# Kernel tuning notes

Hardware: AMD Instinct MI355X
Metric: run time of the kernel (lower is better)

## Reference

```python
import jax, jax.numpy as jnp
import numpy as np

N, F, H, T, E, HOR = 50000, 24, 128, 12, 800000, 6


def setup_inputs() -> dict:
    key = jax.random.key(0)
    ks = jax.random.split(key, 16)
    x_seq = jax.random.normal(ks[0], (T, N, F), jnp.float32)
    ei_seq = jax.random.randint(ks[1], (T, 2, E), 0, N, jnp.int32)
    ea_seq = jax.random.uniform(ks[2], (T, E), jnp.float32)
    mask_seq = jax.random.bernoulli(ks[3], 0.9, (T, N))
    s = 1.0 / float(np.sqrt(H))
    def w(k, shape):
        return jax.random.uniform(k, shape, jnp.float32, -s, s)
    params = dict(
        Wz=w(ks[4], (F, H)), Wr=w(ks[5], (F, H)), Wh=w(ks[6], (F, H)),
        bz=jnp.zeros((H,), jnp.float32), br=jnp.zeros((H,), jnp.float32), bh=jnp.zeros((H,), jnp.float32),
        LWz=w(ks[7], (2 * H, H)), LWr=w(ks[8], (2 * H, H)), LWh=w(ks[9], (2 * H, H)),
        Lbz=w(ks[10], (H,)), Lbr=w(ks[11], (H,)), Lbh=w(ks[12], (H,)),
        headW=w(ks[13], (H, F)), headb=w(ks[14], (F,)),
    )
    return dict(x_seq=x_seq, ei_seq=ei_seq, ea_seq=ea_seq, mask_seq=mask_seq, id_seq=0, **params)


def _gcn(x, src, dst, ew, W, b):
    xw = x @ W                                                     # [N,H]
    deg = jnp.zeros((x.shape[0],), xw.dtype).at[dst].add(ew) + 1.0  # in-degree + self-loop
    dinv = jax.lax.rsqrt(deg)
    coef = dinv[src] * ew * dinv[dst]                              # [E]
    agg = jnp.zeros_like(xw).at[dst].add(xw[src] * coef[:, None])
    return agg + xw * (1.0 / deg)[:, None] + b                     # normalized self-loop term


def _cell(x, src, dst, ew, h, p):
    # TGCN (GCN-GRU) cell from pytorch_geometric_temporal
    z = jax.nn.sigmoid(jnp.concatenate([_gcn(x, src, dst, ew, p['Wz'], p['bz']), h], 1) @ p['LWz'] + p['Lbz'])
    r = jax.nn.sigmoid(jnp.concatenate([_gcn(x, src, dst, ew, p['Wr'], p['br']), h], 1) @ p['LWr'] + p['Lbr'])
    htil = jnp.tanh(jnp.concatenate([_gcn(x, src, dst, ew, p['Wh'], p['bh']), h * r], 1) @ p['LWh'] + p['Lbh'])
    return z * h + (1.0 - z) * htil


def _forward(x_seq, ei_seq, ea_seq, mask_seq, p):
    Nn, Hh = x_seq.shape[1], p['LWz'].shape[1]

    # Encoder over T steps: h_store keeps last hidden of every node ever present
    def enc(carry, inp):
        h_store, seen = carry
        x, ei, ew, mask = inp
        h_prev = jnp.where((mask & seen)[:, None], h_store, 0.0)
        h_new = _cell(x, ei[0], ei[1], ew, h_prev, p)
        return (jnp.where(mask[:, None], h_new, h_store), seen | mask), None

    init = (jnp.zeros((Nn, Hh), x_seq.dtype), jnp.zeros((Nn,), bool))
    (h_store, seen), _ = jax.lax.scan(enc, init, (x_seq, ei_seq, ea_seq, mask_seq))

    h_prev = jnp.where((mask_seq[-1] & seen)[:, None], h_store, 0.0)
    src_l, dst_l, ew_l = ei_seq[-1, 0], ei_seq[-1, 1], ea_seq[-1]

    def dec(carry, _):
        h, inp = carry
        h_new = _cell(inp, src_l, dst_l, ew_l, h, p)
        y = h_new @ p['headW'] + p['headb']
        return (h_new, y), y

    _, preds = jax.lax.scan(dec, (h_prev, x_seq[-1]), None, length=HOR)
    return preds  # [horizon, N, out_channels]


def reference(x_seq, ei_seq, ea_seq, mask_seq, id_seq, Wz, Wr, Wh, bz, br, bh,
              LWz, LWr, LWh, Lbz, Lbr, Lbh, headW, headb):
    p = dict(Wz=Wz, Wr=Wr, Wh=Wh, bz=bz, br=br, bh=bh,
             LWz=LWz, LWr=LWr, LWh=LWh, Lbz=Lbz, Lbr=Lbr, Lbh=Lbh,
             headW=headW, headb=headb)
    return _forward(x_seq, ei_seq, ea_seq, mask_seq, p)
```

## Files before the change

### kernel.cpp

```cpp
#include <hip/hip_runtime.h>

#define NN 50000
#define FF 24
#define HH 128
#define TT 12
#define EE 800000
#define HORZ 6


__global__ void k_maskdetect(const unsigned char* __restrict__ m, int* __restrict__ flag) {
    int i = blockIdx.x * 256 + threadIdx.x;
    if (i < 16384 && (i & 3) != 0 && m[i] != 0) atomicOr(flag, 1);
}

__global__ void k_maskconv(const unsigned char* __restrict__ mraw, const int* __restrict__ flag,
                           unsigned char* __restrict__ mout) {
    int i = blockIdx.x * 256 + threadIdx.x;
    if (i >= TT * NN) return;
    if (*flag) mout[i] = (mraw[i] != 0);
    else       mout[i] = (((const int*)mraw)[i] != 0);
}


__global__ void k_hist(const int* __restrict__ ei, int* __restrict__ cnt,
                       int* __restrict__ rank) {
    int idx = blockIdx.x * 256 + threadIdx.x;
    if (idx >= TT * EE) return;
    int t = idx / EE, e = idx - t * EE;
    int dst = ei[((size_t)t * 2 + 1) * EE + e];
    rank[idx] = atomicAdd(&cnt[t * NN + dst], 1);
}

__global__ void k_scan(const int* __restrict__ cnt, int* __restrict__ offs) {
    __shared__ int sums[1024];
    int t = blockIdx.x, tid = threadIdx.x;
    const int per = (NN + 1023) / 1024;
    int base = tid * per;
    int s = 0;
    for (int i = 0; i < per; i++) {
        int idx = base + i;
        if (idx < NN) s += cnt[t * NN + idx];
    }
    sums[tid] = s;
    __syncthreads();
    for (int off = 1; off < 1024; off <<= 1) {
        int tv = (tid >= off) ? sums[tid - off] : 0;
        __syncthreads();
        sums[tid] += tv;
        __syncthreads();
    }
    int run = sums[tid] - s;
    for (int i = 0; i < per; i++) {
        int idx = base + i;
        if (idx < NN) {
            offs[t * (NN + 1) + idx] = run;
            run += cnt[t * NN + idx];
        }
    }
    if (tid == 1023) offs[t * (NN + 1) + NN] = sums[1023];
}

__global__ void k_fill(const int* __restrict__ ei, const float* __restrict__ ea,
                       const int* __restrict__ offs, const int* __restrict__ rank,
                       int2* __restrict__ edges) {
    int idx = blockIdx.x * 256 + threadIdx.x;
    if (idx >= TT * EE) return;
    int t = idx / EE, e = idx - t * EE;
    int dst = ei[((size_t)t * 2 + 1) * EE + e];
    int src = ei[((size_t)t * 2 + 0) * EE + e];
    int pos = offs[t * (NN + 1) + dst] + rank[idx];
    edges[(size_t)t * EE + pos] = make_int2(src, __float_as_int(ea[(size_t)t * EE + e]));
}

__global__ void k_degdinv(const int* __restrict__ offs, const int2* __restrict__ edges,
                          float* __restrict__ dinv) {
    int idx = blockIdx.x * 256 + threadIdx.x;
    if (idx >= TT * NN) return;
    int t = idx / NN, n = idx - t * NN;
    int b = offs[t * (NN + 1) + n], en = offs[t * (NN + 1) + n + 1];
    float s = 0.f;
    for (int j = b; j < en; j++) s += __int_as_float(edges[(size_t)t * EE + j].y);
    dinv[idx] = rsqrtf(s + 1.0f);
}

__global__ void k_coef(const int* __restrict__ offs, const float* __restrict__ dinv,
                       int2* __restrict__ edges) {
    int idx = blockIdx.x * 256 + threadIdx.x;
    if (idx >= TT * NN) return;
    int t = idx / NN, n = idx - t * NN;
    int b = offs[t * (NN + 1) + n], en = offs[t * (NN + 1) + n + 1];
    float di = dinv[idx];
    for (int j = b; j < en; j++) {
        int2 p = edges[(size_t)t * EE + j];
        float v = __int_as_float(p.y) * di * dinv[t * NN + p.x];
        edges[(size_t)t * EE + j].y = __float_as_int(v);
    }
}


__global__ void k_fold(const float* __restrict__ Wz, const float* __restrict__ Wr,
                       const float* __restrict__ Wh,
                       const float* __restrict__ bz, const float* __restrict__ br,
                       const float* __restrict__ bh,
                       const float* __restrict__ LWz, const float* __restrict__ LWr,
                       const float* __restrict__ LWh,
                       const float* __restrict__ Lbz, const float* __restrict__ Lbr,
                       const float* __restrict__ Lbh,
                       float* __restrict__ Call, float* __restrict__ b2) {
    int g = blockIdx.x, c = threadIdx.x;
    const float* W  = g == 0 ? Wz : (g == 1 ? Wr : Wh);
    const float* LW = g == 0 ? LWz : (g == 1 ? LWr : LWh);
    const float* bg = g == 0 ? bz : (g == 1 ? br : bh);
    const float* Lb = g == 0 ? Lbz : (g == 1 ? Lbr : Lbh);
    for (int j = 0; j < FF; j++) {
        float a = 0.f;
        for (int k = 0; k < HH; k++) a += W[j * HH + k] * LW[k * HH + c];
        Call[((size_t)g * FF + j) * HH + c] = a;
    }
    float a = Lb[c];
    for (int k = 0; k < HH; k++) a += bg[k] * LW[k * HH + c];
    b2[g * HH + c] = a;
}


__global__ void k_gather(const float* __restrict__ x, const int* __restrict__ offs,
                         const int2* __restrict__ edges, const float* __restrict__ dinv,
                         float* __restrict__ xe) {
    int idx = blockIdx.x * 256 + threadIdx.x;
    if (idx >= NN * 6) return;
    int n = idx / 6, q = idx - n * 6;
    int b = offs[n], en = offs[n + 1];
    float di = dinv[n];
    float sc = di * di;
    float4 acc = *(const float4*)&x[(size_t)n * FF + q * 4];
    acc.x *= sc; acc.y *= sc; acc.z *= sc; acc.w *= sc;
    for (int j = b; j < en; j++) {
        int2 p = edges[j];
        float w = __int_as_float(p.y);
        float4 v = *(const float4*)&x[(size_t)p.x * FF + q * 4];
        acc.x += v.x * w; acc.y += v.y * w; acc.z += v.z * w; acc.w += v.w * w;
    }
    *(float4*)&xe[(size_t)n * FF + q * 4] = acc;
}


#define FMA8X2(SARR, M0, K)                                                                  \
    {                                                                                        \
        float4 v_;                                                                           \
        v_ = *(const float4*)&SARR[M0 + 0][K];                                               \
        az0 += v_.x*wz0 + v_.y*wz1 + v_.z*wz2 + v_.w*wz3;                                    \
        ar0 += v_.x*wr0 + v_.y*wr1 + v_.z*wr2 + v_.w*wr3;                                    \
        v_ = *(const float4*)&SARR[M0 + 1][K];                                               \
        az1 += v_.x*wz0 + v_.y*wz1 + v_.z*wz2 + v_.w*wz3;                                    \
        ar1 += v_.x*wr0 + v_.y*wr1 + v_.z*wr2 + v_.w*wr3;                                    \
        v_ = *(const float4*)&SARR[M0 + 2][K];                                               \
        az2 += v_.x*wz0 + v_.y*wz1 + v_.z*wz2 + v_.w*wz3;                                    \
        ar2 += v_.x*wr0 + v_.y*wr1 + v_.z*wr2 + v_.w*wr3;                                    \
        v_ = *(const float4*)&SARR[M0 + 3][K];                                               \
        az3 += v_.x*wz0 + v_.y*wz1 + v_.z*wz2 + v_.w*wz3;                                    \
        ar3 += v_.x*wr0 + v_.y*wr1 + v_.z*wr2 + v_.w*wr3;                                    \
        v_ = *(const float4*)&SARR[M0 + 4][K];                                               \
        az4 += v_.x*wz0 + v_.y*wz1 + v_.z*wz2 + v_.w*wz3;                                    \
        ar4 += v_.x*wr0 + v_.y*wr1 + v_.z*wr2 + v_.w*wr3;                                    \
        v_ = *(const float4*)&SARR[M0 + 5][K];                                               \
        az5 += v_.x*wz0 + v_.y*wz1 + v_.z*wz2 + v_.w*wz3;                                    \
        ar5 += v_.x*wr0 + v_.y*wr1 + v_.z*wr2 + v_.w*wr3;                                    \
        v_ = *(const float4*)&SARR[M0 + 6][K];                                               \
        az6 += v_.x*wz0 + v_.y*wz1 + v_.z*wz2 + v_.w*wz3;                                    \
        ar6 += v_.x*wr0 + v_.y*wr1 + v_.z*wr2 + v_.w*wr3;                                    \
        v_ = *(const float4*)&SARR[M0 + 7][K];                                               \
        az7 += v_.x*wz0 + v_.y*wz1 + v_.z*wz2 + v_.w*wz3;                                    \
        ar7 += v_.x*wr0 + v_.y*wr1 + v_.z*wr2 + v_.w*wr3;                                    \
    }

#define FMA8X(SARR, M0, K)                                                        \
    {                                                                             \
        float4 v_;                                                                \
        v_ = *(const float4*)&SARR[M0 + 0][K]; a0 += v_.x*w0 + v_.y*w1 + v_.z*w2 + v_.w*w3; \
        v_ = *(const float4*)&SARR[M0 + 1][K]; a1 += v_.x*w0 + v_.y*w1 + v_.z*w2 + v_.w*w3; \
        v_ = *(const float4*)&SARR[M0 + 2][K]; a2 += v_.x*w0 + v_.y*w1 + v_.z*w2 + v_.w*w3; \
        v_ = *(const float4*)&SARR[M0 + 3][K]; a3 += v_.x*w0 + v_.y*w1 + v_.z*w2 + v_.w*w3; \
        v_ = *(const float4*)&SARR[M0 + 4][K]; a4 += v_.x*w0 + v_.y*w1 + v_.z*w2 + v_.w*w3; \
        v_ = *(const float4*)&SARR[M0 + 5][K]; a5 += v_.x*w0 + v_.y*w1 + v_.z*w2 + v_.w*w3; \
        v_ = *(const float4*)&SARR[M0 + 6][K]; a6 += v_.x*w0 + v_.y*w1 + v_.z*w2 + v_.w*w3; \
        v_ = *(const float4*)&SARR[M0 + 7][K]; a7 += v_.x*w0 + v_.y*w1 + v_.z*w2 + v_.w*w3; \
    }

template <int DOHEAD>
__global__ __launch_bounds__(256) void k_cell(
        const float* __restrict__ xe, const float* __restrict__ hin,
        const unsigned char* __restrict__ gmask,
        const float* __restrict__ Call, const float* __restrict__ b2,
        const float* __restrict__ LWz, const float* __restrict__ LWr,
        const float* __restrict__ LWh,
        const unsigned char* __restrict__ wmask, float* __restrict__ hout,
        const float* __restrict__ headW, const float* __restrict__ headb,
        float* __restrict__ y) {
    __shared__ float s_xe[16][FF];
    __shared__ float s_h0[16][HH];
    __shared__ float s_z[16][HH];
    __shared__ float s_hr[16][HH];
    int nb = blockIdx.x * 16;
    int tid = threadIdx.x;

    for (int i = tid; i < 16 * FF; i += 256) {
        s_xe[i / FF][i % FF] = xe[(size_t)nb * FF + i];
    }
    for (int i = tid; i < 16 * HH; i += 256) {
        int m = i >> 7, k = i & 127;
        float v = hin[((size_t)nb + m) * HH + k];
        if (gmask && !gmask[nb + m]) v = 0.f;
        s_h0[m][k] = v;
    }
    __syncthreads();

    int g = tid >> 7, c = tid & 127;
    int m0 = g * 8;

    {
        const float* Cz   = Call;
        const float* Cr   = Call + (size_t)FF * HH;
        const float* LWzb = LWz + (size_t)HH * HH;
        const float* LWrb = LWr + (size_t)HH * HH;
        float bbz = b2[c], bbr = b2[HH + c];
        float az0 = bbz, az1 = bbz, az2 = bbz, az3 = bbz, az4 = bbz, az5 = bbz, az6 = bbz, az7 = bbz;
        float ar0 = bbr, ar1 = bbr, ar2 = bbr, ar3 = bbr, ar4 = bbr, ar5 = bbr, ar6 = bbr, ar7 = bbr;
#pragma unroll
        for (int k = 0; k < FF; k += 4) {
            float wz0 = Cz[(k + 0) * HH + c], wz1 = Cz[(k + 1) * HH + c];
            float wz2 = Cz[(k + 2) * HH + c], wz3 = Cz[(k + 3) * HH + c];
            float wr0 = Cr[(k + 0) * HH + c], wr1 = Cr[(k + 1) * HH + c];
            float wr2 = Cr[(k + 2) * HH + c], wr3 = Cr[(k + 3) * HH + c];
            FMA8X2(s_xe, m0, k);
        }
#pragma unroll 4
        for (int k = 0; k < HH; k += 4) {
            float wz0 = LWzb[(k + 0) * HH + c], wz1 = LWzb[(k + 1) * HH + c];
            float wz2 = LWzb[(k + 2) * HH + c], wz3 = LWzb[(k + 3) * HH + c];
            float wr0 = LWrb[(k + 0) * HH + c], wr1 = LWrb[(k + 1) * HH + c];
            float wr2 = LWrb[(k + 2) * HH + c], wr3 = LWrb[(k + 3) * HH + c];
            FMA8X2(s_h0, m0, k);
        }
#pragma unroll
        for (int r = 0; r < 8; r++) {
            float az = (r == 0) ? az0 : (r == 1) ? az1 : (r == 2) ? az2 : (r == 3) ? az3
                     : (r == 4) ? az4 : (r == 5) ? az5 : (r == 6) ? az6 : az7;
            float ar = (r == 0) ? ar0 : (r == 1) ? ar1 : (r == 2) ? ar2 : (r == 3) ? ar3
                     : (r == 4) ? ar4 : (r == 5) ? ar5 : (r == 6) ? ar6 : ar7;
            s_z[m0 + r][c]  = 1.f / (1.f + __expf(-az));
            s_hr[m0 + r][c] = (1.f / (1.f + __expf(-ar))) * s_h0[m0 + r][c];
        }
    }
    __syncthreads();

    {
        const float* Ch   = Call + (size_t)2 * FF * HH;
        const float* LWhb = LWh + (size_t)HH * HH;
        float bb = b2[2 * HH + c];
        float a0 = bb, a1 = bb, a2 = bb, a3 = bb, a4 = bb, a5 = bb, a6 = bb, a7 = bb;
#pragma unroll
        for (int k = 0; k < FF; k += 4) {
            float w0 = Ch[(k + 0) * HH + c], w1 = Ch[(k + 1) * HH + c];
            float w2 = Ch[(k + 2) * HH + c], w3 = Ch[(k + 3) * HH + c];
            FMA8X(s_xe, m0, k);
        }
#pragma unroll 4
        for (int k = 0; k < HH; k += 4) {
            float w0 = LWhb[(k + 0) * HH + c], w1 = LWhb[(k + 1) * HH + c];
            float w2 = LWhb[(k + 2) * HH + c], w3 = LWhb[(k + 3) * HH + c];
            FMA8X(s_hr, m0, k);
        }
#pragma unroll
        for (int r = 0; r < 8; r++) {
            float a = (r == 0) ? a0 : (r == 1) ? a1 : (r == 2) ? a2 : (r == 3) ? a3
                    : (r == 4) ? a4 : (r == 5) ? a5 : (r == 6) ? a6 : a7;
            int m = m0 + r;
            float e2 = __expf(2.f * a);
            float ht = 1.f - 2.f / (e2 + 1.f);
            float z = s_z[m][c];
            float h0v = s_h0[m][c];
            float hn = z * h0v + (1.f - z) * ht;
            int n = nb + m;
            if (wmask) {
                if (wmask[n]) hout[(size_t)n * HH + c] = hn;
            } else {
                hout[(size_t)n * HH + c] = hn;
            }
            if (DOHEAD) s_z[m][c] = hn;
        }
    }

    if (DOHEAD) {
        __syncthreads();
        for (int i = tid; i < 16 * FF; i += 256) {
            int m = i / FF, f = i - m * FF;
            float acc = headb[f];
#pragma unroll 8
            for (int cJ = 0; cJ < HH; cJ++) acc += s_z[m][cJ] * headW[cJ * FF + f];
            y[(size_t)nb * FF + i] = acc;
        }
    }
}

extern "C" void kernel_launch(void* const* d_in, const int* in_sizes, int n_in,
                              void* d_out, int out_size, void* d_ws, size_t ws_size,
                              hipStream_t stream) {
    const float* x_seq = (const float*)d_in[0];
    const int*   ei    = (const int*)d_in[1];
    const float* ea    = (const float*)d_in[2];
    const unsigned char* mraw = (const unsigned char*)d_in[3];
    const float* Wz  = (const float*)d_in[5];
    const float* Wr  = (const float*)d_in[6];
    const float* Wh  = (const float*)d_in[7];
    const float* bz  = (const float*)d_in[8];
    const float* br  = (const float*)d_in[9];
    const float* bh  = (const float*)d_in[10];
    const float* LWz = (const float*)d_in[11];
    const float* LWr = (const float*)d_in[12];
    const float* LWh = (const float*)d_in[13];
    const float* Lbz = (const float*)d_in[14];
    const float* Lbr = (const float*)d_in[15];
    const float* Lbh = (const float*)d_in[16];
    const float* headW = (const float*)d_in[17];
    const float* headb = (const float*)d_in[18];
    float* out = (float*)d_out;

    char* wp = (char*)d_ws;
    int*   cnt    = (int*)wp;   wp += sizeof(int) * TT * NN;
    int*   offs   = (int*)wp;   wp += sizeof(int) * TT * (NN + 1);
    int*   rank   = (int*)wp;   wp += sizeof(int) * (size_t)TT * EE;
    int2*  edges  = (int2*)wp;  wp += sizeof(int2) * (size_t)TT * EE;
    float* dinv   = (float*)wp; wp += sizeof(float) * TT * NN;
    float* hstore = (float*)wp; wp += sizeof(float) * (size_t)NN * HH;
    float* hp     = (float*)wp; wp += sizeof(float) * (size_t)NN * HH;
    float* xebuf  = (float*)wp; wp += sizeof(float) * NN * FF;
    float* Call   = (float*)wp; wp += sizeof(float) * 3 * FF * HH;
    float* b2     = (float*)wp; wp += sizeof(float) * 3 * HH;
    int*   mflag  = (int*)wp;   wp += 256;
    unsigned char* mask = (unsigned char*)wp; wp += TT * NN;
    if (ws_size < (size_t)(wp - (char*)d_ws)) return;

    hipMemsetAsync(mflag, 0, sizeof(int), stream);
    k_maskdetect<<<64, 256, 0, stream>>>(mraw, mflag);
    k_maskconv<<<(TT * NN + 255) / 256, 256, 0, stream>>>(mraw, mflag, mask);

    hipMemsetAsync(cnt, 0, sizeof(int) * TT * NN, stream);
    hipMemsetAsync(hstore, 0, sizeof(float) * NN * HH, stream);
    k_hist<<<(TT * EE + 255) / 256, 256, 0, stream>>>(ei, cnt, rank);
    k_scan<<<TT, 1024, 0, stream>>>(cnt, offs);
    k_fill<<<(TT * EE + 255) / 256, 256, 0, stream>>>(ei, ea, offs, rank, edges);
    k_degdinv<<<(TT * NN + 255) / 256, 256, 0, stream>>>(offs, edges, dinv);
    k_coef<<<(TT * NN + 255) / 256, 256, 0, stream>>>(offs, dinv, edges);
    k_fold<<<3, 128, 0, stream>>>(Wz, Wr, Wh, bz, br, bh, LWz, LWr, LWh, Lbz, Lbr, Lbh, Call, b2);

    for (int t = 0; t < TT; t++) {
        const float* xt = x_seq + (size_t)t * NN * FF;
        const unsigned char* mt = mask + (size_t)t * NN;
        k_gather<<<(NN * 6 + 255) / 256, 256, 0, stream>>>(
            xt, offs + t * (NN + 1), edges + (size_t)t * EE, dinv + t * NN, xebuf);
        k_cell<0><<<NN / 16, 256, 0, stream>>>(
            xebuf, hstore, mt, Call, b2, LWz, LWr, LWh, mt, hstore,
            nullptr, nullptr, nullptr);
    }

    const int*  offsl  = offs + (TT - 1) * (NN + 1);
    const int2* edgesl = edges + (size_t)(TT - 1) * EE;
    const float* dil   = dinv + (TT - 1) * NN;
    for (int k = 0; k < HORZ; k++) {
        const float* xin = (k == 0) ? (x_seq + (size_t)(TT - 1) * NN * FF)
                                    : (out + (size_t)(k - 1) * NN * FF);
        k_gather<<<(NN * 6 + 255) / 256, 256, 0, stream>>>(
            xin, offsl, edgesl, dil, xebuf);
        k_cell<1><<<NN / 16, 256, 0, stream>>>(
            xebuf, (k == 0) ? hstore : hp,
            (k == 0) ? (mask + (size_t)(TT - 1) * NN) : nullptr,
            Call, b2, LWz, LWr, LWh, nullptr, hp,
            headW, headb, out + (size_t)k * NN * FF);
    }
}
```

Measured before the change: 4.398 ms.

## Retile GRU cell kernel to 2 rows x 4 columns per thread with float4 weights

Changes the per-thread work split in the GRU cell kernel from 8 rows by 1 column to 2 rows by 4 contiguous columns. Weight loads become float4 and z gates stay in registers instead of a shared array, which shrinks shared memory and removes a store/reload. The intent is to cut global weight load instructions and LDS traffic. The trade-off is less weight reuse per load across rows (2 instead of 8), so L1/L2 weight traffic per node roughly quadruples.

Result: slower. 4.930 ms (+12.1%).

```diff
diff --git a/kernel.cpp b/kernel.cpp
--- a/kernel.cpp
+++ b/kernel.cpp
@@ -6,6 +6,27 @@
 #define TT 12
 #define EE 800000
 #define HORZ 6
+#define BR 16
+
+__device__ __forceinline__ void fma4(float4& a, float s, const float4& w) {
+    a.x += s * w.x; a.y += s * w.y; a.z += s * w.z; a.w += s * w.w;
+}
+__device__ __forceinline__ float4 sig4(float4 a) {
+    float4 r;
+    r.x = 1.f / (1.f + __expf(-a.x));
+    r.y = 1.f / (1.f + __expf(-a.y));
+    r.z = 1.f / (1.f + __expf(-a.z));
+    r.w = 1.f / (1.f + __expf(-a.w));
+    return r;
+}
+__device__ __forceinline__ float4 tanh4(float4 a) {
+    float4 r;
+    r.x = 1.f - 2.f / (__expf(2.f * a.x) + 1.f);
+    r.y = 1.f - 2.f / (__expf(2.f * a.y) + 1.f);
+    r.z = 1.f - 2.f / (__expf(2.f * a.z) + 1.f);
+    r.w = 1.f - 2.f / (__expf(2.f * a.w) + 1.f);
+    return r;
+}
 
 
 __global__ void k_maskdetect(const unsigned char* __restrict__ m, int* __restrict__ flag) {
@@ -144,48 +165,6 @@
 }
 
 
-#define FMA8X2(SARR, M0, K)                                                                  \
-    {                                                                                        \
-        float4 v_;                                                                           \
-        v_ = *(const float4*)&SARR[M0 + 0][K];                                               \
-        az0 += v_.x*wz0 + v_.y*wz1 + v_.z*wz2 + v_.w*wz3;                                    \
-        ar0 += v_.x*wr0 + v_.y*wr1 + v_.z*wr2 + v_.w*wr3;                                    \
-        v_ = *(const float4*)&SARR[M0 + 1][K];                                               \
-        az1 += v_.x*wz0 + v_.y*wz1 + v_.z*wz2 + v_.w*wz3;                                    \
-        ar1 += v_.x*wr0 + v_.y*wr1 + v_.z*wr2 + v_.w*wr3;                                    \
-        v_ = *(const float4*)&SARR[M0 + 2][K];                                               \
-        az2 += v_.x*wz0 + v_.y*wz1 + v_.z*wz2 + v_.w*wz3;                                    \
-        ar2 += v_.x*wr0 + v_.y*wr1 + v_.z*wr2 + v_.w*wr3;                                    \
-        v_ = *(const float4*)&SARR[M0 + 3][K];                                               \
-        az3 += v_.x*wz0 + v_.y*wz1 + v_.z*wz2 + v_.w*wz3;                                    \
-        ar3 += v_.x*wr0 + v_.y*wr1 + v_.z*wr2 + v_.w*wr3;                                    \
-        v_ = *(const float4*)&SARR[M0 + 4][K];                                               \
-        az4 += v_.x*wz0 + v_.y*wz1 + v_.z*wz2 + v_.w*wz3;                                    \
-        ar4 += v_.x*wr0 + v_.y*wr1 + v_.z*wr2 + v_.w*wr3;                                    \
-        v_ = *(const float4*)&SARR[M0 + 5][K];                                               \
-        az5 += v_.x*wz0 + v_.y*wz1 + v_.z*wz2 + v_.w*wz3;                                    \
-        ar5 += v_.x*wr0 + v_.y*wr1 + v_.z*wr2 + v_.w*wr3;                                    \
-        v_ = *(const float4*)&SARR[M0 + 6][K];                                               \
-        az6 += v_.x*wz0 + v_.y*wz1 + v_.z*wz2 + v_.w*wz3;                                    \
-        ar6 += v_.x*wr0 + v_.y*wr1 + v_.z*wr2 + v_.w*wr3;                                    \
-        v_ = *(const float4*)&SARR[M0 + 7][K];                                               \
-        az7 += v_.x*wz0 + v_.y*wz1 + v_.z*wz2 + v_.w*wz3;                                    \
-        ar7 += v_.x*wr0 + v_.y*wr1 + v_.z*wr2 + v_.w*wr3;                                    \
-    }
-
-#define FMA8X(SARR, M0, K)                                                        \
-    {                                                                             \
-        float4 v_;                                                                \
-        v_ = *(const float4*)&SARR[M0 + 0][K]; a0 += v_.x*w0 + v_.y*w1 + v_.z*w2 + v_.w*w3; \
-        v_ = *(const float4*)&SARR[M0 + 1][K]; a1 += v_.x*w0 + v_.y*w1 + v_.z*w2 + v_.w*w3; \
-        v_ = *(const float4*)&SARR[M0 + 2][K]; a2 += v_.x*w0 + v_.y*w1 + v_.z*w2 + v_.w*w3; \
-        v_ = *(const float4*)&SARR[M0 + 3][K]; a3 += v_.x*w0 + v_.y*w1 + v_.z*w2 + v_.w*w3; \
-        v_ = *(const float4*)&SARR[M0 + 4][K]; a4 += v_.x*w0 + v_.y*w1 + v_.z*w2 + v_.w*w3; \
-        v_ = *(const float4*)&SARR[M0 + 5][K]; a5 += v_.x*w0 + v_.y*w1 + v_.z*w2 + v_.w*w3; \
-        v_ = *(const float4*)&SARR[M0 + 6][K]; a6 += v_.x*w0 + v_.y*w1 + v_.z*w2 + v_.w*w3; \
-        v_ = *(const float4*)&SARR[M0 + 7][K]; a7 += v_.x*w0 + v_.y*w1 + v_.z*w2 + v_.w*w3; \
-    }
-
 template <int DOHEAD>
 __global__ __launch_bounds__(256) void k_cell(
         const float* __restrict__ xe, const float* __restrict__ hin,
@@ -196,17 +175,16 @@
         const unsigned char* __restrict__ wmask, float* __restrict__ hout,
         const float* __restrict__ headW, const float* __restrict__ headb,
         float* __restrict__ y) {
-    __shared__ float s_xe[16][FF];
-    __shared__ float s_h0[16][HH];
-    __shared__ float s_z[16][HH];
-    __shared__ float s_hr[16][HH];
-    int nb = blockIdx.x * 16;
+    __shared__ float s_xe[BR][FF];
+    __shared__ float s_h0[BR][HH];
+    __shared__ float s_hr[BR][HH];
+    int nb = blockIdx.x * BR;
     int tid = threadIdx.x;
 
-    for (int i = tid; i < 16 * FF; i += 256) {
+    for (int i = tid; i < BR * FF; i += 256) {
         s_xe[i / FF][i % FF] = xe[(size_t)nb * FF + i];
     }
-    for (int i = tid; i < 16 * HH; i += 256) {
+    for (int i = tid; i < BR * HH; i += 256) {
         int m = i >> 7, k = i & 127;
         float v = hin[((size_t)nb + m) * HH + k];
         if (gmask && !gmask[nb + m]) v = 0.f;
@@ -214,89 +192,125 @@
     }
     __syncthreads();
 
-    int g = tid >> 7, c = tid & 127;
-    int m0 = g * 8;
+    int c4 = (tid & 31) * 4;
+    int m0 = (tid >> 5) * 2;
+
+    float4 zz0, zz1;
 
     {
         const float* Cz   = Call;
         const float* Cr   = Call + (size_t)FF * HH;
         const float* LWzb = LWz + (size_t)HH * HH;
         const float* LWrb = LWr + (size_t)HH * HH;
-        float bbz = b2[c], bbr = b2[HH + c];
-        float az0 = bbz, az1 = bbz, az2 = bbz, az3 = bbz, az4 = bbz, az5 = bbz, az6 = bbz, az7 = bbz;
-        float ar0 = bbr, ar1 = bbr, ar2 = bbr, ar3 = bbr, ar4 = bbr, ar5 = bbr, ar6 = bbr, ar7 = bbr;
+        float4 bz4 = *(const float4*)&b2[c4];
+        float4 br4 = *(const float4*)&b2[HH + c4];
+        float4 az0 = bz4, az1 = bz4, ar0 = br4, ar1 = br4;
 #pragma unroll
         for (int k = 0; k < FF; k += 4) {
-            float wz0 = Cz[(k + 0) * HH + c], wz1 = Cz[(k + 1) * HH + c];
-            float wz2 = Cz[(k + 2) * HH + c], wz3 = Cz[(k + 3) * HH + c];
-            float wr0 = Cr[(k + 0) * HH + c], wr1 = Cr[(k + 1) * HH + c];
-            float wr2 = Cr[(k + 2) * HH + c], wr3 = Cr[(k + 3) * HH + c];
-            FMA8X2(s_xe, m0, k);
+            float4 wz0 = *(const float4*)&Cz[(k + 0) * HH + c4];
+            float4 wz1 = *(const float4*)&Cz[(k + 1) * HH + c4];
+            float4 wz2 = *(const float4*)&Cz[(k + 2) * HH + c4];
+            float4 wz3 = *(const float4*)&Cz[(k + 3) * HH + c4];
+            float4 wr0 = *(const float4*)&Cr[(k + 0) * HH + c4];
+            float4 wr1 = *(const float4*)&Cr[(k + 1) * HH + c4];
+            float4 wr2 = *(const float4*)&Cr[(k + 2) * HH + c4];
+            float4 wr3 = *(const float4*)&Cr[(k + 3) * HH + c4];
+            float4 v0 = *(const float4*)&s_xe[m0 + 0][k];
+            float4 v1 = *(const float4*)&s_xe[m0 + 1][k];
+            fma4(az0, v0.x, wz0); fma4(az0, v0.y, wz1); fma4(az0, v0.z, wz2); fma4(az0, v0.w, wz3);
+            fma4(az1, v1.x, wz0); fma4(az1, v1.y, wz1); fma4(az1, v1.z, wz2); fma4(az1, v1.w, wz3);
+            fma4(ar0, v0.x, wr0); fma4(ar0, v0.y, wr1); fma4(ar0, v0.z, wr2); fma4(ar0, v0.w, wr3);
+            fma4(ar1, v1.x, wr0); fma4(ar1, v1.y, wr1); fma4(ar1, v1.z, wr2); fma4(ar1, v1.w, wr3);
         }
 #pragma unroll 4
         for (int k = 0; k < HH; k += 4) {
-            float wz0 = LWzb[(k + 0) * HH + c], wz1 = LWzb[(k + 1) * HH + c];
-            float wz2 = LWzb[(k + 2) * HH + c], wz3 = LWzb[(k + 3) * HH + c];
-            float wr0 = LWrb[(k + 0) * HH + c], wr1 = LWrb[(k + 1) * HH + c];
-            float wr2 = LWrb[(k + 2) * HH + c], wr3 = LWrb[(k + 3) * HH + c];
-            FMA8X2(s_h0, m0, k);
-        }
-#pragma unroll
-        for (int r = 0; r < 8; r++) {
-            float az = (r == 0) ? az0 : (r == 1) ? az1 : (r == 2) ? az2 : (r == 3) ? az3
-                     : (r == 4) ? az4 : (r == 5) ? az5 : (r == 6) ? az6 : az7;
-            float ar = (r == 0) ? ar0 : (r == 1) ? ar1 : (r == 2) ? ar2 : (r == 3) ? ar3
-                     : (r == 4) ? ar4 : (r == 5) ? ar5 : (r == 6) ? ar6 : ar7;
-            s_z[m0 + r][c]  = 1.f / (1.f + __expf(-az));
-            s_hr[m0 + r][c] = (1.f / (1.f + __expf(-ar))) * s_h0[m0 + r][c];
-        }
+            float4 wz0 = *(const float4*)&LWzb[(k + 0) * HH + c4];
+            float4 wz1 = *(const float4*)&LWzb[(k + 1) * HH + c4];
+            float4 wz2 = *(const float4*)&LWzb[(k + 2) * HH + c4];
+            float4 wz3 = *(const float4*)&LWzb[(k + 3) * HH + c4];
+            float4 wr0 = *(const float4*)&LWrb[(k + 0) * HH + c4];
+            float4 wr1 = *(const float4*)&LWrb[(k + 1) * HH + c4];
+            float4 wr2 = *(const float4*)&LWrb[(k + 2) * HH + c4];
+            float4 wr3 = *(const float4*)&LWrb[(k + 3) * HH + c4];
+            float4 v0 = *(const float4*)&s_h0[m0 + 0][k];
+            float4 v1 = *(const float4*)&s_h0[m0 + 1][k];
+            fma4(az0, v0.x, wz0); fma4(az0, v0.y, wz1); fma4(az0, v0.z, wz2); fma4(az0, v0.w, wz3);
+            fma4(az1, v1.x, wz0); fma4(az1, v1.y, wz1); fma4(az1, v1.z, wz2); fma4(az1, v1.w, wz3);
+            fma4(ar0, v0.x, wr0); fma4(ar0, v0.y, wr1); fma4(ar0, v0.z, wr2); fma4(ar0, v0.w, wr3);
+            fma4(ar1, v1.x, wr0); fma4(ar1, v1.y, wr1); fma4(ar1, v1.z, wr2); fma4(ar1, v1.w, wr3);
+        }
+        zz0 = sig4(az0);
+        zz1 = sig4(az1);
+        float4 s0 = sig4(ar0), s1 = sig4(ar1);
+        float4 h00 = *(const float4*)&s_h0[m0 + 0][c4];
+        float4 h01 = *(const float4*)&s_h0[m0 + 1][c4];
+        float4 hr0, hr1;
+        hr0.x = s0.x * h00.x; hr0.y = s0.y * h00.y; hr0.z = s0.z * h00.z; hr0.w = s0.w * h00.w;
+        hr1.x = s1.x * h01.x; hr1.y = s1.y * h01.y; hr1.z = s1.z * h01.z; hr1.w = s1.w * h01.w;
+        *(float4*)&s_hr[m0 + 0][c4] = hr0;
+        *(float4*)&s_hr[m0 + 1][c4] = hr1;
     }
     __syncthreads();
 
     {
         const float* Ch   = Call + (size_t)2 * FF * HH;
         const float* LWhb = LWh + (size_t)HH * HH;
-        float bb = b2[2 * HH + c];
-        float a0 = bb, a1 = bb, a2 = bb, a3 = bb, a4 = bb, a5 = bb, a6 = bb, a7 = bb;
+        float4 bh4 = *(const float4*)&b2[2 * HH + c4];
+        float4 ah0 = bh4, ah1 = bh4;
 #pragma unroll
         for (int k = 0; k < FF; k += 4) {
-            float w0 = Ch[(k + 0) * HH + c], w1 = Ch[(k + 1) * HH + c];
-            float w2 = Ch[(k + 2) * HH + c], w3 = Ch[(k + 3) * HH + c];
-            FMA8X(s_xe, m0, k);
+            float4 w0 = *(const float4*)&Ch[(k + 0) * HH + c4];
+            float4 w1 = *(const float4*)&Ch[(k + 1) * HH + c4];
+            float4 w2 = *(const float4*)&Ch[(k + 2) * HH + c4];
+            float4 w3 = *(const float4*)&Ch[(k + 3) * HH + c4];
+            float4 v0 = *(const float4*)&s_xe[m0 + 0][k];
+            float4 v1 = *(const float4*)&s_xe[m0 + 1][k];
+            fma4(ah0, v0.x, w0); fma4(ah0, v0.y, w1); fma4(ah0, v0.z, w2); fma4(ah0, v0.w, w3);
+            fma4(ah1, v1.x, w0); fma4(ah1, v1.y, w1); fma4(ah1, v1.z, w2); fma4(ah1, v1.w, w3);
         }
 #pragma unroll 4
         for (int k = 0; k < HH; k += 4) {
-            float w0 = LWhb[(k + 0) * HH + c], w1 = LWhb[(k + 1) * HH + c];
-            float w2 = LWhb[(k + 2) * HH + c], w3 = LWhb[(k + 3) * HH + c];
-            FMA8X(s_hr, m0, k);
-        }
-#pragma unroll
-        for (int r = 0; r < 8; r++) {
-            float a = (r == 0) ? a0 : (r == 1) ? a1 : (r == 2) ? a2 : (r == 3) ? a3
-                    : (r == 4) ? a4 : (r == 5) ? a5 : (r == 6) ? a6 : a7;
-            int m = m0 + r;
-            float e2 = __expf(2.f * a);
-            float ht = 1.f - 2.f / (e2 + 1.f);
-            float z = s_z[m][c];
-            float h0v = s_h0[m][c];
-            float hn = z * h0v + (1.f - z) * ht;
-            int n = nb + m;
-            if (wmask) {
-                if (wmask[n]) hout[(size_t)n * HH + c] = hn;
-            } else {
-                hout[(size_t)n * HH + c] = hn;
-            }
-            if (DOHEAD) s_z[m][c] = hn;
+            float4 w0 = *(const float4*)&LWhb[(k + 0) * HH + c4];
+            float4 w1 = *(const float4*)&LWhb[(k + 1) * HH + c4];
+            float4 w2 = *(const float4*)&LWhb[(k + 2) * HH + c4];
+            float4 w3 = *(const float4*)&LWhb[(k + 3) * HH + c4];
+            float4 v0 = *(const float4*)&s_hr[m0 + 0][k];
+            float4 v1 = *(const float4*)&s_hr[m0 + 1][k];
+            fma4(ah0, v0.x, w0); fma4(ah0, v0.y, w1); fma4(ah0, v0.z, w2); fma4(ah0, v0.w, w3);
+            fma4(ah1, v1.x, w0); fma4(ah1, v1.y, w1); fma4(ah1, v1.z, w2); fma4(ah1, v1.w, w3);
+        }
+        float4 ht0 = tanh4(ah0), ht1 = tanh4(ah1);
+        float4 h00 = *(const float4*)&s_h0[m0 + 0][c4];
+        float4 h01 = *(const float4*)&s_h0[m0 + 1][c4];
+        float4 hn0, hn1;
+        hn0.x = zz0.x * h00.x + (1.f - zz0.x) * ht0.x;
+        hn0.y = zz0.y * h00.y + (1.f - zz0.y) * ht0.y;
+        hn0.z = zz0.z * h00.z + (1.f - zz0.z) * ht0.z;
+        hn0.w = zz0.w * h00.w + (1.f - zz0.w) * ht0.w;
+        hn1.x = zz1.x * h01.x + (1.f - zz1.x) * ht1.x;
+        hn1.y = zz1.y * h01.y + (1.f - zz1.y) * ht1.y;
+        hn1.z = zz1.z * h01.z + (1.f - zz1.z) * ht1.z;
+        hn1.w = zz1.w * h01.w + (1.f - zz1.w) * ht1.w;
+        int n0 = nb + m0, n1 = nb + m0 + 1;
+        if (!wmask || wmask[n0]) *(float4*)&hout[(size_t)n0 * HH + c4] = hn0;
+        if (!wmask || wmask[n1]) *(float4*)&hout[(size_t)n1 * HH + c4] = hn1;
+        if (DOHEAD) {
+            *(float4*)&s_h0[m0 + 0][c4] = hn0;
+            *(float4*)&s_h0[m0 + 1][c4] = hn1;
         }
     }
 
     if (DOHEAD) {
         __syncthreads();
-        for (int i = tid; i < 16 * FF; i += 256) {
+        for (int i = tid; i < BR * FF; i += 256) {
             int m = i / FF, f = i - m * FF;
             float acc = headb[f];
 #pragma unroll 8
-            for (int cJ = 0; cJ < HH; cJ++) acc += s_z[m][cJ] * headW[cJ * FF + f];
+            for (int cJ = 0; cJ < HH; cJ += 4) {
+                float4 hv = *(const float4*)&s_h0[m][cJ];
+                acc += hv.x * headW[(cJ + 0) * FF + f] + hv.y * headW[(cJ + 1) * FF + f]
+                     + hv.z * headW[(cJ + 2) * FF + f] + hv.w * headW[(cJ + 3) * FF + f];
+            }
             y[(size_t)nb * FF + i] = acc;
         }
     }
@@ -358,7 +372,7 @@
         const unsigned char* mt = mask + (size_t)t * NN;
         k_gather<<<(NN * 6 + 255) / 256, 256, 0, stream>>>(
             xt, offs + t * (NN + 1), edges + (size_t)t * EE, dinv + t * NN, xebuf);
-        k_cell<0><<<NN / 16, 256, 0, stream>>>(
+        k_cell<0><<<NN / BR, 256, 0, stream>>>(
             xebuf, hstore, mt, Call, b2, LWz, LWr, LWh, mt, hstore,
             nullptr, nullptr, nullptr);
     }
@@ -371,7 +385,7 @@
                                     : (out + (size_t)(k - 1) * NN * FF);
         k_gather<<<(NN * 6 + 255) / 256, 256, 0, stream>>>(
             xin, offsl, edgesl, dil, xebuf);
-        k_cell<1><<<NN / 16, 256, 0, stream>>>(
+        k_cell<1><<<NN / BR, 256, 0, stream>>>(
             xebuf, (k == 0) ? hstore : hp,
             (k == 0) ? (mask + (size_t)(TT - 1) * NN) : nullptr,
             Call, b2, LWz, LWr, LWh, nullptr, hp,
```

## Batch encoder graph gathers into one launch and reuse last-step gather

Applied to the files above, without the earlier changes.

All twelve encoder-step neighbour gathers of x are independent of the hidden state, so they are computed in a single large kernel into a per-step buffer before the recurrent cell loop. The workspace aliases this buffer with the rank/count scratch, which is dead by then. The first decoder step reuses the last encoder gather instead of recomputing it. This cuts launch count and gives the gather more parallelism per launch, at the cost of a larger workspace and a fallback path when the workspace is too small.

New measurement: 4.278 ms, median of 2. -2.7%, faster.

```diff
diff --git a/kernel.cpp b/kernel.cpp
--- a/kernel.cpp
+++ b/kernel.cpp
@@ -123,12 +123,11 @@
 }
 
 
-__global__ void k_gather(const float* __restrict__ x, const int* __restrict__ offs,
-                         const int2* __restrict__ edges, const float* __restrict__ dinv,
-                         float* __restrict__ xe) {
-    int idx = blockIdx.x * 256 + threadIdx.x;
-    if (idx >= NN * 6) return;
-    int n = idx / 6, q = idx - n * 6;
+__device__ __forceinline__ void gather_body(int n, int q, const float* __restrict__ x,
+                                            const int* __restrict__ offs,
+                                            const int2* __restrict__ edges,
+                                            const float* __restrict__ dinv,
+                                            float* __restrict__ xe) {
     int b = offs[n], en = offs[n + 1];
     float di = dinv[n];
     float sc = di * di;
@@ -141,6 +140,31 @@
         acc.x += v.x * w; acc.y += v.y * w; acc.z += v.z * w; acc.w += v.w * w;
     }
     *(float4*)&xe[(size_t)n * FF + q * 4] = acc;
+}
+
+__global__ void k_gather(const float* __restrict__ x, const int* __restrict__ offs,
+                         const int2* __restrict__ edges, const float* __restrict__ dinv,
+                         float* __restrict__ xe) {
+    int idx = blockIdx.x * 256 + threadIdx.x;
+    if (idx >= NN * 6) return;
+    int n = idx / 6, q = idx - n * 6;
+    gather_body(n, q, x, offs, edges, dinv, xe);
+}
+
+__global__ void k_gather12(const float* __restrict__ x_seq, const int* __restrict__ offs_all,
+                           const int2* __restrict__ edges_all, const float* __restrict__ dinv_all,
+                           float* __restrict__ xe_all) {
+    int idx = blockIdx.x * 256 + threadIdx.x;
+    if (idx >= TT * NN * 6) return;
+    int t = idx / (NN * 6);
+    int r = idx - t * (NN * 6);
+    int n = r / 6, q = r - n * 6;
+    gather_body(n, q,
+                x_seq + (size_t)t * NN * FF,
+                offs_all + t * (NN + 1),
+                edges_all + (size_t)t * EE,
+                dinv_all + t * NN,
+                xe_all + (size_t)t * NN * FF);
 }
 
 
@@ -325,20 +349,35 @@
     const float* headb = (const float*)d_in[18];
     float* out = (float*)d_out;
 
+    const size_t sz_rankcnt = sizeof(int) * (size_t)TT * EE + sizeof(int) * TT * NN;
+    const size_t sz_xe1  = sizeof(float) * (size_t)NN * FF;
+    const size_t sz_xe12 = sz_xe1 * TT;
+    const size_t regA_big   = (sz_xe12 > sz_rankcnt) ? sz_xe12 : sz_rankcnt;
+    const size_t regA_small = (sz_xe1  > sz_rankcnt) ? sz_xe1  : sz_rankcnt;
+    const size_t sz_rest = sizeof(int) * TT * (NN + 1)
+                         + sizeof(int2) * (size_t)TT * EE
+                         + sizeof(float) * TT * NN
+                         + sizeof(float) * (size_t)NN * HH * 2
+                         + sizeof(float) * (3 * FF * HH + 3 * HH)
+                         + 256 + TT * NN + 1024;
+    bool batched = (ws_size >= regA_big + sz_rest);
+    size_t regA = batched ? regA_big : regA_small;
+    if (!batched && ws_size < regA_small + sz_rest) return;
+
     char* wp = (char*)d_ws;
-    int*   cnt    = (int*)wp;   wp += sizeof(int) * TT * NN;
+    int*   rank   = (int*)wp;
+    int*   cnt    = (int*)(wp + sizeof(int) * (size_t)TT * EE);
+    float* xebuf  = (float*)wp;
+    wp += regA;
     int*   offs   = (int*)wp;   wp += sizeof(int) * TT * (NN + 1);
-    int*   rank   = (int*)wp;   wp += sizeof(int) * (size_t)TT * EE;
     int2*  edges  = (int2*)wp;  wp += sizeof(int2) * (size_t)TT * EE;
     float* dinv   = (float*)wp; wp += sizeof(float) * TT * NN;
     float* hstore = (float*)wp; wp += sizeof(float) * (size_t)NN * HH;
     float* hp     = (float*)wp; wp += sizeof(float) * (size_t)NN * HH;
-    float* xebuf  = (float*)wp; wp += sizeof(float) * NN * FF;
     float* Call   = (float*)wp; wp += sizeof(float) * 3 * FF * HH;
     float* b2     = (float*)wp; wp += sizeof(float) * 3 * HH;
     int*   mflag  = (int*)wp;   wp += 256;
-    unsigned char* mask = (unsigned char*)wp; wp += TT * NN;
-    if (ws_size < (size_t)(wp - (char*)d_ws)) return;
+    unsigned char* mask = (unsigned char*)wp;
 
     hipMemsetAsync(mflag, 0, sizeof(int), stream);
     k_maskdetect<<<64, 256, 0, stream>>>(mraw, mflag);
@@ -353,28 +392,56 @@
     k_coef<<<(TT * NN + 255) / 256, 256, 0, stream>>>(offs, dinv, edges);
     k_fold<<<3, 128, 0, stream>>>(Wz, Wr, Wh, bz, br, bh, LWz, LWr, LWh, Lbz, Lbr, Lbh, Call, b2);
 
-    for (int t = 0; t < TT; t++) {
-        const float* xt = x_seq + (size_t)t * NN * FF;
-        const unsigned char* mt = mask + (size_t)t * NN;
-        k_gather<<<(NN * 6 + 255) / 256, 256, 0, stream>>>(
-            xt, offs + t * (NN + 1), edges + (size_t)t * EE, dinv + t * NN, xebuf);
-        k_cell<0><<<NN / 16, 256, 0, stream>>>(
-            xebuf, hstore, mt, Call, b2, LWz, LWr, LWh, mt, hstore,
-            nullptr, nullptr, nullptr);
-    }
-
     const int*  offsl  = offs + (TT - 1) * (NN + 1);
     const int2* edgesl = edges + (size_t)(TT - 1) * EE;
     const float* dil   = dinv + (TT - 1) * NN;
-    for (int k = 0; k < HORZ; k++) {
-        const float* xin = (k == 0) ? (x_seq + (size_t)(TT - 1) * NN * FF)
-                                    : (out + (size_t)(k - 1) * NN * FF);
-        k_gather<<<(NN * 6 + 255) / 256, 256, 0, stream>>>(
-            xin, offsl, edgesl, dil, xebuf);
-        k_cell<1><<<NN / 16, 256, 0, stream>>>(
-            xebuf, (k == 0) ? hstore : hp,
-            (k == 0) ? (mask + (size_t)(TT - 1) * NN) : nullptr,
-            Call, b2, LWz, LWr, LWh, nullptr, hp,
-            headW, headb, out + (size_t)k * NN * FF);
-    }
-}
+
+    if (batched) {
+        k_gather12<<<(TT * NN * 6 + 255) / 256, 256, 0, stream>>>(
+            x_seq, offs, edges, dinv, xebuf);
+
+        for (int t = 0; t < TT; t++) {
+            const unsigned char* mt = mask + (size_t)t * NN;
+            k_cell<0><<<NN / 16, 256, 0, stream>>>(
+                xebuf + (size_t)t * NN * FF, hstore, mt, Call, b2, LWz, LWr, LWh, mt, hstore,
+                nullptr, nullptr, nullptr);
+        }
+
+        for (int k = 0; k < HORZ; k++) {
+            const float* xek;
+            if (k == 0) {
+                xek = xebuf + (size_t)(TT - 1) * NN * FF;
+            } else {
+                k_gather<<<(NN * 6 + 255) / 256, 256, 0, stream>>>(
+                    out + (size_t)(k - 1) * NN * FF, offsl, edgesl, dil, xebuf);
+                xek = xebuf;
+            }
+            k_cell<1><<<NN / 16, 256, 0, stream>>>(
+                xek, (k == 0) ? hstore : hp,
+                (k == 0) ? (mask + (size_t)(TT - 1) * NN) : nullptr,
+                Call, b2, LWz, LWr, LWh, nullptr, hp,
+                headW, headb, out + (size_t)k * NN * FF);
+        }
+    } else {
+        for (int t = 0; t < TT; t++) {
+            const unsigned char* mt = mask + (size_t)t * NN;
+            k_gather<<<(NN * 6 + 255) / 256, 256, 0, stream>>>(
+                x_seq + (size_t)t * NN * FF, offs + t * (NN + 1),
+                edges + (size_t)t * EE, dinv + t * NN, xebuf);
+            k_cell<0><<<NN / 16, 256, 0, stream>>>(
+                xebuf, hstore, mt, Call, b2, LWz, LWr, LWh, mt, hstore,
+                nullptr, nullptr, nullptr);
+        }
+        for (int k = 0; k < HORZ; k++) {
+            const float* xin = (k == 0) ? (x_seq + (size_t)(TT - 1) * NN * FF)
+                                        : (out + (size_t)(k - 1) * NN * FF);
+            k_gather<<<(NN * 6 + 255) / 256, 256, 0, stream>>>(
+                xin, offsl, edgesl, dil, xebuf);
+            k_cell<1><<<NN / 16, 256, 0, stream>>>(
+                xebuf, (k == 0) ? hstore : hp,
+                (k == 0) ? (mask + (size_t)(TT - 1) * NN) : nullptr,
+                Call, b2, LWz, LWr, LWh, nullptr, hp,
+                headW, headb, out + (size_t)k * NN * FF);
+        }
+    }
+}
```
